# Optimization experiments

Measured on AMD Instinct MI355X. Metric: run time of the kernel, lower is better.

Reference implementation:

```python
import jax, jax.numpy as jnp
import numpy as np

N = 16384      # nodes
E = 65536      # edges
G = 512        # graphs in batch
F_NODE = 9
F_EDGE = 3
H = 64         # hidden_dim
H2 = 32        # hidden_dim // 2
HEADS = 2
DIMS = [(64, 64), (64, 64), (64, 32)]  # (in_dim, out_dim) per NNConv layer
EPS = 1e-5


def setup_inputs() -> dict:
    keys = iter(jax.random.split(jax.random.key(0), 64))

    def nrm(shape, scale=0.05):
        return jax.random.normal(next(keys), shape, jnp.float32) * scale

    inp = {}
    inp["x"] = nrm((N, F_NODE), 1.0)
    src = jax.random.randint(next(keys), (E,), 0, N)
    dst = jax.random.randint(next(keys), (E,), 0, N)
    inp["edge_index"] = jnp.stack([src, dst]).astype(jnp.int32)
    inp["edge_attr"] = nrm((E, F_EDGE), 1.0)
    inp["batch"] = jnp.sort(jax.random.randint(next(keys), (N,), 0, G)).astype(jnp.int32)
    inp["ee_w"] = nrm((F_EDGE, H2)); inp["ee_b"] = nrm((H2,))
    inp["ne_w"] = nrm((F_NODE, H)); inp["ne_b"] = nrm((H,))
    for i, (din, dout) in enumerate(DIMS):
        inp[f"m{i}_w1"] = nrm((H2, H * HEADS)); inp[f"m{i}_b1"] = nrm((H * HEADS,))
        inp[f"m{i}_w2"] = nrm((H * HEADS, din * dout)); inp[f"m{i}_b2"] = nrm((din * dout,))
        inp[f"root{i}"] = nrm((din, dout)); inp[f"cb{i}"] = nrm((dout,))
        inp[f"bn{i}_g"] = jnp.ones((dout,), jnp.float32)
        inp[f"bn{i}_b"] = jnp.zeros((dout,), jnp.float32)
    inp["fc_w"] = nrm((H2, 12)); inp["fc_b"] = nrm((12,))
    return inp


def reference(x, edge_index, edge_attr, batch, ee_w, ee_b, ne_w, ne_b,
              m0_w1, m0_b1, m0_w2, m0_b2, root0, cb0, bn0_g, bn0_b,
              m1_w1, m1_b1, m1_w2, m1_b2, root1, cb1, bn1_g, bn1_b,
              m2_w1, m2_b1, m2_w2, m2_b2, root2, cb2, bn2_g, bn2_b,
              fc_w, fc_b):
    src, dst = edge_index[0], edge_index[1]
    ee = edge_attr @ ee_w + ee_b                 # [E, H2] edge embedding
    h = x @ ne_w + ne_b                          # [N, H] node embedding
    layers = [(m0_w1, m0_b1, m0_w2, m0_b2, root0, cb0, bn0_g, bn0_b),
              (m1_w1, m1_b1, m1_w2, m1_b2, root1, cb1, bn1_g, bn1_b),
              (m2_w1, m2_b1, m2_w2, m2_b2, root2, cb2, bn2_g, bn2_b)]
    deg = jnp.maximum(jax.ops.segment_sum(jnp.ones((E, 1), h.dtype), dst, num_segments=N), 1.0)
    for i, (w1, b1, w2, b2, root, cb, g, bb) in enumerate(layers):
        din, dout = DIMS[i]
        ew = jax.nn.relu(ee @ w1 + b1)           # [E, H*HEADS] edge MLP hidden
        W = (ew @ w2 + b2).reshape(E, din, dout) # per-edge weight matrices
        msg = jnp.einsum('ei,eio->eo', h[src], W)  # gather + per-edge matvec
        aggr = jax.ops.segment_sum(msg, dst, num_segments=N) / deg  # scatter-mean
        h = h @ root + aggr + cb                 # NNConv root weight + bias
        mean = h.mean(0); var = h.var(0)         # BatchNorm1d (batch stats)
        h = jax.nn.relu(g * (h - mean) * jax.lax.rsqrt(var + EPS) + bb)
        # dropout skipped (eval / deterministic reference)
    cnt = jnp.maximum(jax.ops.segment_sum(jnp.ones((N, 1), h.dtype), batch, num_segments=G), 1.0)
    pooled = jax.ops.segment_sum(h, batch, num_segments=G) / cnt  # global_mean_pool
    return jax.nn.sigmoid(pooled @ fc_w + fc_b)
```

## Files before the change

kernel.cpp:

```cpp
#include <hip/hip_runtime.h>
#include <hip/hip_bf16.h>
#include <math.h>

constexpr int NN = 16384;
constexpr int NE = 65536;
constexpr int NG = 512;

typedef __attribute__((ext_vector_type(8)))  short short8;
typedef __attribute__((ext_vector_type(16))) float f32x16;

__device__ __forceinline__ short f2bf(float f) {
    unsigned u = __builtin_bit_cast(unsigned, f);
    return (short)((u + 0x7FFFu + ((u >> 16) & 1u)) >> 16);
}
__device__ __forceinline__ float b2f(unsigned short s) {
    return __builtin_bit_cast(float, (unsigned)s << 16);
}
__device__ __forceinline__ void gload_lds16(const unsigned short* g, unsigned short* l) {
    __builtin_amdgcn_global_load_lds(
        (const __attribute__((address_space(1))) unsigned int*)g,
        (__attribute__((address_space(3))) unsigned int*)l, 16, 0, 0);
}

__device__ __forceinline__ short8 agen(const float* h, float e) {
    unsigned u[4];
#pragma unroll
    for (int q = 0; q < 4; q++) {
        float2 p; p.x = h[2 * q] * e; p.y = h[2 * q + 1] * e;
        __hip_bfloat162 b = __float22bfloat162_rn(p);
        unsigned v; __builtin_memcpy(&v, &b, 4);
        u[q] = v;
    }
    uint4 uv = make_uint4(u[0], u[1], u[2], u[3]);
    return __builtin_bit_cast(short8, uv);
}

__global__ void k_nh(const float* __restrict__ x, const float* __restrict__ w,
                     const float* __restrict__ b, float* __restrict__ h,
                     unsigned short* __restrict__ hbf) {
    int idx = blockIdx.x * 256 + threadIdx.x;
    int n = idx >> 6, o = idx & 63;
    const float* xr = x + n * 9;
    float s = b[o];
#pragma unroll
    for (int a = 0; a < 9; a++) s += xr[a] * w[a * 64 + o];
    h[idx] = s;
    hbf[idx] = (unsigned short)f2bf(s);
}

__global__ void k_deg(const int* __restrict__ ei, float* __restrict__ deg) {
    int e = blockIdx.x * 256 + threadIdx.x;
    atomicAdd(&deg[ei[NE + e]], 1.0f);
}

__global__ __launch_bounds__(256) void k_ewt(const float* __restrict__ ea,
                                             const float* __restrict__ eew,
                                             const float* __restrict__ eeb,
                                             const float* __restrict__ w1,
                                             const float* __restrict__ b1,
                                             unsigned short* __restrict__ ewT) {
    __shared__ float w1s[32 * 128];
    __shared__ float b1s[128];
    __shared__ float eews[96], eebs[32];
    int t = threadIdx.x;
    for (int c = t; c < 4096; c += 256) w1s[c] = w1[c];
    if (t < 128) b1s[t] = b1[t];
    if (t < 96)  eews[t] = eew[t];
    if (t < 32)  eebs[t] = eeb[t];
    __syncthreads();

    int e = blockIdx.x * 64 + (t & 63);
    int w = t >> 6;
    float a0 = ea[e * 3], a1 = ea[e * 3 + 1], a2 = ea[e * 3 + 2];
    float eer[32];
#pragma unroll
    for (int j = 0; j < 32; j++)
        eer[j] = eebs[j] + a0 * eews[j] + a1 * eews[32 + j] + a2 * eews[64 + j];
    float acc[32];
#pragma unroll
    for (int c = 0; c < 32; c++) acc[c] = b1s[w * 32 + c];
    for (int j = 0; j < 32; j++) {
        float ej = eer[j];
#pragma unroll
        for (int c = 0; c < 32; c++) acc[c] += ej * w1s[j * 128 + w * 32 + c];
    }
#pragma unroll
    for (int c = 0; c < 32; c++) {
        float v = fmaxf(acc[c], 0.f);
        ewT[(size_t)(w * 32 + c) * NE + e] = (unsigned short)f2bf(v);
    }
}

template <int DOUT>
__global__ void k_packw2(const float* __restrict__ w2, const float* __restrict__ b2,
                         unsigned short* __restrict__ w2p) {
    constexpr int TILES = DOUT / 32;
    int idx = blockIdx.x * 256 + threadIdx.x;
    int j = idx & 7, l = (idx >> 3) & 63;
    int rest = idx >> 9;
    int tt = rest % TILES;
    int s  = (rest / TILES) & 3;
    int kc = rest / (4 * TILES);
    int i = s * 16 + (l >> 5) * 8 + j;
    int o = tt * 32 + (l & 31);
    float v = (kc < 128) ? w2[(size_t)kc * 64 * DOUT + i * DOUT + o]
                         : (kc == 128 ? b2[i * DOUT + o] : 0.f);
    w2p[idx] = (unsigned short)f2bf(v);
}

template <int DOUT>
__global__ __launch_bounds__(128, 1) void k_msg_mfma(const int* __restrict__ ei,
                                                     const unsigned short* __restrict__ hbf,
                                                     const unsigned short* __restrict__ ewT,
                                                     const unsigned short* __restrict__ w2p,
                                                     float* __restrict__ aggr) {
    constexpr int TILES = DOUT / 32;
    constexpr int SL    = 4 * TILES * 64 * 8;
    constexpr int CH    = 2;
    constexpr int CHSL  = CH * SL;
    constexpr int NCH   = 66;
    __shared__ __align__(16) unsigned short w2s[2 * CHSL];
    __shared__ __align__(16) unsigned short ews[136 * 128];

    int t = threadIdx.x;
    int w = t >> 6, l = t & 63;
    int hi = l >> 5, ln = l & 31;
    int eb = blockIdx.x * 128;
    int ew0 = w * 64;

#pragma unroll
    for (int i = 0; i < 17; i++) {
        int row = i * 8 + (t >> 4);
        int rowc = row < 128 ? row : 127;
        gload_lds16(ewT + (size_t)rowc * NE + eb + (t & 15) * 8,
                    ews + i * 1024 + t * 8);
    }
#pragma unroll
    for (int p = 0; p < CHSL / 1024; p++)
        gload_lds16(w2p + p * 1024 + t * 8, w2s + p * 1024 + t * 8);

    float hf[2][4][8];
#pragma unroll
    for (int m = 0; m < 2; m++) {
        int sidx = ei[eb + ew0 + m * 32 + ln];
        const unsigned short* hrow = hbf + (size_t)sidx * 64;
#pragma unroll
        for (int s = 0; s < 4; s++) {
            short8 hv = *(const short8*)(hrow + (s * 2 + hi) * 8);
#pragma unroll
            for (int j = 0; j < 8; j++) hf[m][s][j] = b2f((unsigned short)hv[j]);
        }
    }

    f32x16 acc[2][TILES];
#pragma unroll
    for (int m = 0; m < 2; m++)
#pragma unroll
        for (int tt = 0; tt < TILES; tt++)
#pragma unroll
            for (int r = 0; r < 16; r++) acc[m][tt][r] = 0.f;

    __syncthreads();

    for (int c = 0; c < NCH; c++) {
        if (c + 1 < NCH) {
            const unsigned short* g = w2p + (size_t)(c + 1) * CHSL;
            unsigned short* ld = w2s + ((c + 1) & 1) * CHSL;
#pragma unroll
            for (int p = 0; p < CHSL / 1024; p++)
                gload_lds16(g + p * 1024 + t * 8, ld + p * 1024 + t * 8);
        }
        const unsigned short* cbuf = w2s + (c & 1) * CHSL;
#pragma unroll
        for (int s2 = 0; s2 < CH; s2++) {
            int kc = c * CH + s2;
            float r0 = b2f(ews[kc * 128 + ew0 + ln]);
            float r1 = b2f(ews[kc * 128 + ew0 + 32 + ln]);
            float ewc0 = (kc < 128) ? r0 : (kc == 128 ? 1.f : 0.f);
            float ewc1 = (kc < 128) ? r1 : (kc == 128 ? 1.f : 0.f);
            const unsigned short* sbuf = cbuf + s2 * SL;
#pragma unroll
            for (int s = 0; s < 4; s++) {
                short8 a0 = agen(hf[0][s], ewc0);
                short8 a1 = agen(hf[1][s], ewc1);
#pragma unroll
                for (int tt = 0; tt < TILES; tt++) {
                    short8 b = *(const short8*)(sbuf + ((s * TILES + tt) * 64 + l) * 8);
                    acc[0][tt] = __builtin_amdgcn_mfma_f32_32x32x16_bf16(a0, b, acc[0][tt], 0, 0, 0);
                    acc[1][tt] = __builtin_amdgcn_mfma_f32_32x32x16_bf16(a1, b, acc[1][tt], 0, 0, 0);
                }
            }
        }
        __syncthreads();
    }

#pragma unroll
    for (int m = 0; m < 2; m++)
#pragma unroll
        for (int r = 0; r < 16; r++) {
            int row = (r & 3) + 8 * (r >> 2) + 4 * hi;
            int d = ei[NE + eb + ew0 + m * 32 + row];
#pragma unroll
            for (int tt = 0; tt < TILES; tt++)
                atomicAdd(&aggr[(size_t)d * DOUT + tt * 32 + ln], acc[m][tt][r]);
        }
}

template <int DOUT>
__global__ void k_combine(const float* __restrict__ h, const float* __restrict__ root,
                          const float* __restrict__ aggr, const float* __restrict__ deg,
                          const float* __restrict__ cb, float* __restrict__ htmp) {
    int idx = blockIdx.x * 256 + threadIdx.x;
    int n = idx / DOUT, o = idx % DOUT;
    const float* hr = h + n * 64;
    float s = cb[o] + aggr[idx] / fmaxf(deg[n], 1.f);
#pragma unroll 8
    for (int i = 0; i < 64; i++) s += hr[i] * root[i * DOUT + o];
    htmp[idx] = s;
}

template <int DOUT>
__global__ void k_bnstats(const float* __restrict__ htmp, float* __restrict__ sums) {
    int o = blockIdx.x >> 3, chunk = blockIdx.x & 7, t = threadIdx.x;
    float s = 0.f, q = 0.f;
    int n0 = chunk * (NN / 8);
    for (int n = n0 + t; n < n0 + NN / 8; n += 256) {
        float v = htmp[n * DOUT + o];
        s += v; q += v * v;
    }
    for (int off = 32; off; off >>= 1) { s += __shfl_down(s, off); q += __shfl_down(q, off); }
    __shared__ float ls[4], lq[4];
    int w = t >> 6;
    if ((t & 63) == 0) { ls[w] = s; lq[w] = q; }
    __syncthreads();
    if (t == 0) {
        s = ls[0] + ls[1] + ls[2] + ls[3];
        q = lq[0] + lq[1] + lq[2] + lq[3];
        atomicAdd(&sums[o], s);
        atomicAdd(&sums[DOUT + o], q);
    }
}

template <int DOUT>
__global__ void k_bnfinal(const float* __restrict__ sums, const float* __restrict__ g,
                          const float* __restrict__ bb, float* __restrict__ scale,
                          float* __restrict__ shift) {
    int o = threadIdx.x;
    if (o < DOUT) {
        float mean = sums[o] / NN;
        float var  = sums[DOUT + o] / NN - mean * mean;
        float sc   = g[o] * rsqrtf(var + 1e-5f);
        scale[o] = sc;
        shift[o] = bb[o] - mean * sc;
    }
}

template <int DOUT, bool WB>
__global__ void k_bnapply(const float* __restrict__ htmp, const float* __restrict__ scale,
                          const float* __restrict__ shift, float* __restrict__ hout,
                          unsigned short* __restrict__ hbf) {
    int idx = blockIdx.x * 256 + threadIdx.x;
    int o = idx & (DOUT - 1);
    float v = fmaxf(htmp[idx] * scale[o] + shift[o], 0.f);
    hout[idx] = v;
    if (WB) hbf[idx] = (unsigned short)f2bf(v);
}

__global__ void k_pool(const float* __restrict__ h, const int* __restrict__ batch,
                       float* __restrict__ pool, float* __restrict__ cnt) {
    int idx = blockIdx.x * 256 + threadIdx.x;
    int n = idx >> 5, o = idx & 31;
    int b = batch[n];
    atomicAdd(&pool[b * 32 + o], h[idx]);
    if (o == 0) atomicAdd(&cnt[b], 1.0f);
}

__global__ void k_fc(const float* __restrict__ pool, const float* __restrict__ cnt,
                     const float* __restrict__ w, const float* __restrict__ b,
                     float* __restrict__ out) {
    int idx = blockIdx.x * 256 + threadIdx.x;
    int gI = idx / 12, t = idx % 12;
    float inv = 1.f / fmaxf(cnt[gI], 1.f);
    float s = 0.f;
#pragma unroll 8
    for (int j = 0; j < 32; j++) s += pool[gI * 32 + j] * w[j * 12 + t];
    s = s * inv + b[t];
    out[idx] = 1.f / (1.f + expf(-s));
}

extern "C" void kernel_launch(void* const* d_in, const int* in_sizes, int n_in,
                              void* d_out, int out_size, void* d_ws, size_t ws_size,
                              hipStream_t stream) {
    const float* x   = (const float*)d_in[0];
    const int*   ei  = (const int*)d_in[1];
    const float* ea  = (const float*)d_in[2];
    const int*   bat = (const int*)d_in[3];
    const float* eew = (const float*)d_in[4];
    const float* eeb = (const float*)d_in[5];
    const float* nw  = (const float*)d_in[6];
    const float* nb  = (const float*)d_in[7];
    const float* fcw = (const float*)d_in[32];
    const float* fcb = (const float*)d_in[33];
    float* out = (float*)d_out;

    char* ws = (char*)d_ws;
    unsigned short* ewT = (unsigned short*)(ws + 0);
    unsigned short* w2p = (unsigned short*)(ws + 16777216);
    float* hA    = (float*)(ws + 18874368);
    float* hB    = (float*)(ws + 23068672);
    float* htmp  = (float*)(ws + 27262976);
    float* aggr  = (float*)(ws + 31457280);
    float* sums  = (float*)(ws + 35651584);
    unsigned short* hbf = (unsigned short*)(ws + 35652608);
    float* deg   = (float*)(ws + 37749760);
    float* scale = (float*)(ws + 37815296);
    float* shift = (float*)(ws + 37815552);
    float* pool  = (float*)(ws + 37815808);
    float* cnt   = (float*)(ws + 37881344);

    (void)hipMemsetAsync(deg, 0, NN * 4, stream);
    (void)hipMemsetAsync(pool, 0, NG * 32 * 4 + NG * 4, stream);

    k_nh<<<NN * 64 / 256, 256, 0, stream>>>(x, nw, nb, hA, hbf);
    k_deg<<<NE / 256, 256, 0, stream>>>(ei, deg);

    float* hin = hA;
    float* hout = hB;
    for (int L = 0; L < 3; L++) {
        const float* w1 = (const float*)d_in[8 + 8 * L + 0];
        const float* b1 = (const float*)d_in[8 + 8 * L + 1];
        const float* w2 = (const float*)d_in[8 + 8 * L + 2];
        const float* b2 = (const float*)d_in[8 + 8 * L + 3];
        const float* rt = (const float*)d_in[8 + 8 * L + 4];
        const float* cb = (const float*)d_in[8 + 8 * L + 5];
        const float* bg = (const float*)d_in[8 + 8 * L + 6];
        const float* bb = (const float*)d_in[8 + 8 * L + 7];

        (void)hipMemsetAsync(aggr, 0, NN * 64 * 4 + 1024, stream);

        k_ewt<<<NE / 64, 256, 0, stream>>>(ea, eew, eeb, w1, b1, ewT);

        if (L < 2) {
            k_packw2<64><<<132 * 4096 / 256, 256, 0, stream>>>(w2, b2, w2p);
            k_msg_mfma<64><<<NE / 128, 128, 0, stream>>>(ei, hbf, ewT, w2p, aggr);
            k_combine<64><<<NN * 64 / 256, 256, 0, stream>>>(hin, rt, aggr, deg, cb, htmp);
            k_bnstats<64><<<64 * 8, 256, 0, stream>>>(htmp, sums);
            k_bnfinal<64><<<1, 64, 0, stream>>>(sums, bg, bb, scale, shift);
            k_bnapply<64, true><<<NN * 64 / 256, 256, 0, stream>>>(htmp, scale, shift, hout, hbf);
        } else {
            k_packw2<32><<<132 * 2048 / 256, 256, 0, stream>>>(w2, b2, w2p);
            k_msg_mfma<32><<<NE / 128, 128, 0, stream>>>(ei, hbf, ewT, w2p, aggr);
            k_combine<32><<<NN * 32 / 256, 256, 0, stream>>>(hin, rt, aggr, deg, cb, htmp);
            k_bnstats<32><<<32 * 8, 256, 0, stream>>>(htmp, sums);
            k_bnfinal<32><<<1, 64, 0, stream>>>(sums, bg, bb, scale, shift);
            k_bnapply<32, false><<<NN * 32 / 256, 256, 0, stream>>>(htmp, scale, shift, hout, hbf);
        }
        float* tmp = hin; hin = hout; hout = tmp;
    }
    k_pool<<<NN * 32 / 256, 256, 0, stream>>>(hin, bat, pool, cnt);
    k_fc<<<NG * 12 / 256, 256, 0, stream>>>(pool, cnt, fcw, fcb, out);
}
```

Before: 627.8 us.

## Split message MFMA kernel into four waves of 32 edges per block

Reworks the per-edge message kernel so each 128-edge block uses four waves, each computing one 32-edge MFMA tile instead of two waves computing two tiles each. This halves accumulator and h-fragment registers per wave and raises launch bounds to 256 threads with 2 blocks per CU to improve latency hiding. Cooperative LDS staging loops are re-strided for 256 threads. In exchange, each LDS B-fragment load now feeds one MFMA instead of two, increasing LDS traffic per MFMA.

```diff
diff --git a/kernel.cpp b/kernel.cpp
--- a/kernel.cpp
+++ b/kernel.cpp
@@ -109,7 +109,7 @@
 }
 
 template <int DOUT>
-__global__ __launch_bounds__(128, 1) void k_msg_mfma(const int* __restrict__ ei,
+__global__ __launch_bounds__(256, 2) void k_msg_mfma(const int* __restrict__ ei,
                                                      const unsigned short* __restrict__ hbf,
                                                      const unsigned short* __restrict__ ewT,
                                                      const unsigned short* __restrict__ w2p,
@@ -120,45 +120,43 @@
     constexpr int CHSL  = CH * SL;
     constexpr int NCH   = 66;
     __shared__ __align__(16) unsigned short w2s[2 * CHSL];
-    __shared__ __align__(16) unsigned short ews[136 * 128];
+    __shared__ __align__(16) unsigned short ews[144 * 128];
 
     int t = threadIdx.x;
     int w = t >> 6, l = t & 63;
     int hi = l >> 5, ln = l & 31;
     int eb = blockIdx.x * 128;
-    int ew0 = w * 64;
-
-#pragma unroll
-    for (int i = 0; i < 17; i++) {
-        int row = i * 8 + (t >> 4);
+    int e0 = w * 32;
+
+#pragma unroll
+    for (int i = 0; i < 9; i++) {
+        int idx = i * 256 + t;
+        int row = idx >> 4;
         int rowc = row < 128 ? row : 127;
-        gload_lds16(ewT + (size_t)rowc * NE + eb + (t & 15) * 8,
-                    ews + i * 1024 + t * 8);
-    }
-#pragma unroll
-    for (int p = 0; p < CHSL / 1024; p++)
-        gload_lds16(w2p + p * 1024 + t * 8, w2s + p * 1024 + t * 8);
-
-    float hf[2][4][8];
-#pragma unroll
-    for (int m = 0; m < 2; m++) {
-        int sidx = ei[eb + ew0 + m * 32 + ln];
+        gload_lds16(ewT + (size_t)rowc * NE + eb + (idx & 15) * 8,
+                    ews + idx * 8);
+    }
+#pragma unroll
+    for (int p = 0; p < CHSL / 2048; p++)
+        gload_lds16(w2p + p * 2048 + t * 8, w2s + p * 2048 + t * 8);
+
+    float hf[4][8];
+    {
+        int sidx = ei[eb + e0 + ln];
         const unsigned short* hrow = hbf + (size_t)sidx * 64;
 #pragma unroll
         for (int s = 0; s < 4; s++) {
             short8 hv = *(const short8*)(hrow + (s * 2 + hi) * 8);
 #pragma unroll
-            for (int j = 0; j < 8; j++) hf[m][s][j] = b2f((unsigned short)hv[j]);
+            for (int j = 0; j < 8; j++) hf[s][j] = b2f((unsigned short)hv[j]);
         }
     }
 
-    f32x16 acc[2][TILES];
-#pragma unroll
-    for (int m = 0; m < 2; m++)
-#pragma unroll
-        for (int tt = 0; tt < TILES; tt++)
-#pragma unroll
-            for (int r = 0; r < 16; r++) acc[m][tt][r] = 0.f;
+    f32x16 acc[TILES];
+#pragma unroll
+    for (int tt = 0; tt < TILES; tt++)
+#pragma unroll
+        for (int r = 0; r < 16; r++) acc[tt][r] = 0.f;
 
     __syncthreads();
 
@@ -167,27 +165,23 @@
             const unsigned short* g = w2p + (size_t)(c + 1) * CHSL;
             unsigned short* ld = w2s + ((c + 1) & 1) * CHSL;
 #pragma unroll
-            for (int p = 0; p < CHSL / 1024; p++)
-                gload_lds16(g + p * 1024 + t * 8, ld + p * 1024 + t * 8);
+            for (int p = 0; p < CHSL / 2048; p++)
+                gload_lds16(g + p * 2048 + t * 8, ld + p * 2048 + t * 8);
         }
         const unsigned short* cbuf = w2s + (c & 1) * CHSL;
 #pragma unroll
         for (int s2 = 0; s2 < CH; s2++) {
             int kc = c * CH + s2;
-            float r0 = b2f(ews[kc * 128 + ew0 + ln]);
-            float r1 = b2f(ews[kc * 128 + ew0 + 32 + ln]);
-            float ewc0 = (kc < 128) ? r0 : (kc == 128 ? 1.f : 0.f);
-            float ewc1 = (kc < 128) ? r1 : (kc == 128 ? 1.f : 0.f);
+            float rv = b2f(ews[kc * 128 + e0 + ln]);
+            float ewc = (kc < 128) ? rv : (kc == 128 ? 1.f : 0.f);
             const unsigned short* sbuf = cbuf + s2 * SL;
 #pragma unroll
             for (int s = 0; s < 4; s++) {
-                short8 a0 = agen(hf[0][s], ewc0);
-                short8 a1 = agen(hf[1][s], ewc1);
+                short8 a = agen(hf[s], ewc);
 #pragma unroll
                 for (int tt = 0; tt < TILES; tt++) {
                     short8 b = *(const short8*)(sbuf + ((s * TILES + tt) * 64 + l) * 8);
-                    acc[0][tt] = __builtin_amdgcn_mfma_f32_32x32x16_bf16(a0, b, acc[0][tt], 0, 0, 0);
-                    acc[1][tt] = __builtin_amdgcn_mfma_f32_32x32x16_bf16(a1, b, acc[1][tt], 0, 0, 0);
+                    acc[tt] = __builtin_amdgcn_mfma_f32_32x32x16_bf16(a, b, acc[tt], 0, 0, 0);
                 }
             }
         }
@@ -195,15 +189,13 @@
     }
 
 #pragma unroll
-    for (int m = 0; m < 2; m++)
-#pragma unroll
-        for (int r = 0; r < 16; r++) {
-            int row = (r & 3) + 8 * (r >> 2) + 4 * hi;
-            int d = ei[NE + eb + ew0 + m * 32 + row];
-#pragma unroll
-            for (int tt = 0; tt < TILES; tt++)
-                atomicAdd(&aggr[(size_t)d * DOUT + tt * 32 + ln], acc[m][tt][r]);
-        }
+    for (int r = 0; r < 16; r++) {
+        int row = (r & 3) + 8 * (r >> 2) + 4 * hi;
+        int d = ei[NE + eb + e0 + row];
+#pragma unroll
+        for (int tt = 0; tt < TILES; tt++)
+            atomicAdd(&aggr[(size_t)d * DOUT + tt * 32 + ln], acc[tt][r]);
+    }
 }
 
 template <int DOUT>
@@ -342,14 +334,14 @@
 
         if (L < 2) {
             k_packw2<64><<<132 * 4096 / 256, 256, 0, stream>>>(w2, b2, w2p);
-            k_msg_mfma<64><<<NE / 128, 128, 0, stream>>>(ei, hbf, ewT, w2p, aggr);
+            k_msg_mfma<64><<<NE / 128, 256, 0, stream>>>(ei, hbf, ewT, w2p, aggr);
             k_combine<64><<<NN * 64 / 256, 256, 0, stream>>>(hin, rt, aggr, deg, cb, htmp);
             k_bnstats<64><<<64 * 8, 256, 0, stream>>>(htmp, sums);
             k_bnfinal<64><<<1, 64, 0, stream>>>(sums, bg, bb, scale, shift);
             k_bnapply<64, true><<<NN * 64 / 256, 256, 0, stream>>>(htmp, scale, shift, hout, hbf);
         } else {
             k_packw2<32><<<132 * 2048 / 256, 256, 0, stream>>>(w2, b2, w2p);
-            k_msg_mfma<32><<<NE / 128, 128, 0, stream>>>(ei, hbf, ewT, w2p, aggr);
+            k_msg_mfma<32><<<NE / 128, 256, 0, stream>>>(ei, hbf, ewT, w2p, aggr);
             k_combine<32><<<NN * 32 / 256, 256, 0, stream>>>(hin, rt, aggr, deg, cb, htmp);
             k_bnstats<32><<<32 * 8, 256, 0, stream>>>(htmp, sums);
             k_bnfinal<32><<<1, 64, 0, stream>>>(sums, bg, bb, scale, shift);
```

After: 514.4 us. 18.1% less time.
